# Performance work log

Hardware: AMD Instinct MI355X
Metric: run time of the kernel (lower is better)

## Reference

```python
import jax, jax.numpy as jnp
import numpy as np

DIM = 300
VOCAB = 50000
B = 16
T_ART = 2000   # divisible by lcm(1,2,4,10,25)=100 -> no remainder branch in ContractExpand
T_Q = 30
T_OPT = 16
RANGES = (1, 2, 4, 10, 25)


def setup_inputs():
    key = jax.random.key(0)
    ks = jax.random.split(key, 32)
    s = 1.0 / np.sqrt(DIM)
    n = lambda i, shape, scale: jax.random.normal(ks[i], shape, jnp.float32) * scale
    return {
        "option1_in": jax.random.randint(ks[0], (B, T_OPT), 0, VOCAB),
        "option2_in": jax.random.randint(ks[1], (B, T_OPT), 0, VOCAB),
        "option3_in": jax.random.randint(ks[2], (B, T_OPT), 0, VOCAB),
        "option4_in": jax.random.randint(ks[3], (B, T_OPT), 0, VOCAB),
        "question_in": jax.random.randint(ks[4], (B, T_Q), 0, VOCAB),
        "article_in": jax.random.randint(ks[5], (B, T_ART), 0, VOCAB),
        "emb": n(6, (VOCAB, DIM), 0.1),
        # ContractExpand: 5 range-specific DIM->DIM linears
        "ce_W": n(7, (5, DIM, DIM), s),
        "ce_b": n(8, (5, DIM), 0.01),
        # MultiRangedReasoning gate mixers: 5->3 and 3->1
        "mr1_W": n(9, (3, 5), 0.4),
        "mr1_b": n(10, (3,), 0.01),
        "mr2_W": n(11, (1, 3), 0.05),   # small scale keeps gate < 1 so 2000-step scan is stable
        "mr2_b": jnp.zeros((1,), jnp.float32),
        # MRU encoding linears
        "Wz": n(12, (DIM, DIM), s), "bz": n(13, (DIM,), 0.01),
        "Wo": n(14, (DIM, DIM), s), "bo": n(15, (DIM,), 0.01),
        # BiAttention key projections
        "f1_W": n(16, (DIM, DIM), s), "f1_b": n(17, (DIM,), 0.01),
        "f2_W": n(18, (DIM, DIM), s), "f2_b": n(19, (DIM,), 0.01),
        "f3_W": n(20, (DIM, DIM), s), "f3_b": n(21, (DIM,), 0.01),
        # AnswerSelection: 2*DIM -> DIM/4 -> 1
        "as1_W": n(22, (DIM // 4, 2 * DIM), 1.0 / np.sqrt(2 * DIM)),
        "as1_b": n(23, (DIM // 4,), 0.01),
        "as2_W": n(24, (1, DIM // 4), 1.0 / np.sqrt(DIM // 4)),
        "as2_b": n(25, (1,), 0.01),
    }


def _attention(main, attn_in, W, b):
    # score[b,t,w] = (W @ attn_in[b,w] + b) . main[b,t]; softmax over w; mix attn_in
    keys = attn_in @ W.T + b                               # (B,Tw,D)
    probs = jax.nn.softmax(jnp.einsum('btd,bwd->btw', main, keys), axis=-1)
    return jnp.einsum('btw,bwd->btd', probs, attn_in)      # (B,Tt,D)


def _forward(option1_in, option2_in, option3_in, option4_in, question_in, article_in,
             emb, ce_W, ce_b, mr1_W, mr1_b, mr2_W, mr2_b, Wz, bz, Wo, bo,
             f1_W, f1_b, f2_W, f2_b, f3_W, f3_b, as1_W, as1_b, as2_W, as2_b):
    art = emb[article_in]                                  # (B,T,D)
    q = emb[question_in]                                   # (B,Tq,D)
    opts = [emb[o] for o in (option1_in, option2_in, option3_in, option4_in)]

    # --- MultiRangedReasoning gate ---
    blocks = []
    for i, r in enumerate(RANGES):
        g = T_ART // r
        xs = art.reshape(B, g, r, DIM).sum(2)              # group-sum over r consecutive words
        h = jax.nn.relu(jnp.einsum('bgd,ed->bge', xs, ce_W[i]) + ce_b[i])
        blocks.append(jnp.repeat(h, r, axis=1) / r)        # expand back to (B,T,D)
    Y = jnp.stack(blocks, axis=-1)                         # (B,T,D,5)
    h1 = jax.nn.relu(jnp.einsum('btdr,kr->btdk', Y, mr1_W) + mr1_b)
    gate = jax.nn.relu(jnp.einsum('btdk,ok->btdo', h1, mr2_W) + mr2_b)[..., 0]  # (B,T,D)

    # --- MRU encoding: c_t = g_t*c_{t-1} + (1-g_t)*z_t ; h_t = o_t*c_t ---
    z = jnp.tanh(art @ Wz.T + bz)
    o = jnp.tanh(art @ Wo.T + bo)

    def step(c, gz):
        g_t, z_t = gz
        c = g_t * c + (1.0 - g_t) * z_t
        return c, c

    _, cs = jax.lax.scan(step, jnp.zeros((B, DIM), art.dtype),
                         (gate.transpose(1, 0, 2), z.transpose(1, 0, 2)))
    art_enc = o * cs.transpose(1, 0, 2)                    # (B,T,D)

    # --- bi-attention + per-option answer vector ---
    aoq = _attention(art_enc, q, f1_W, f1_b)               # article on question
    vecs = []
    for opt in opts:
        aoqo = _attention(aoq, opt, f2_W, f2_b)            # (B,T,D)
        ooa = _attention(aoq, opt, f3_W, f3_b)             # (B,T,D)
        vecs.append(jnp.concatenate([aoqo.mean(1), ooa.mean(1)], axis=-1))  # (B,2D)
    ans = jnp.stack(vecs, 0)                               # (4,B,2D)

    h = jax.nn.relu(ans @ as1_W.T + as1_b)                 # (4,B,75)
    scores = (h @ as2_W.T + as2_b)[..., 0]                 # (4,B)
    return scores.T                                        # (B,4)


def reference(option1_in, option2_in, option3_in, option4_in, question_in, article_in,
              emb, ce_W, ce_b, mr1_W, mr1_b, mr2_W, mr2_b, Wz, bz, Wo, bo,
              f1_W, f1_b, f2_W, f2_b, f3_W, f3_b, as1_W, as1_b, as2_W, as2_b):
    return _forward(option1_in, option2_in, option3_in, option4_in, question_in, article_in,
                    emb, ce_W, ce_b, mr1_W, mr1_b, mr2_W, mr2_b, Wz, bz, Wo, bo,
                    f1_W, f1_b, f2_W, f2_b, f3_W, f3_b, as1_W, as1_b, as2_W, as2_b)
```

## Files before the change

### kernel.cpp

```cpp
#include <hip/hip_runtime.h>
#include <math.h>

typedef unsigned short ushortT;
typedef short bf8 __attribute__((ext_vector_type(8)));
typedef float f32x4 __attribute__((ext_vector_type(4)));
typedef unsigned short us4 __attribute__((ext_vector_type(4)));

__device__ __forceinline__ float bf2f(ushortT u){
    union { unsigned int i; float f; } v; v.i = ((unsigned int)u) << 16; return v.f;
}
__device__ __forceinline__ ushortT f2bf(float f){
    union { float f; unsigned int i; } v; v.f = f;
    unsigned int x = v.i;
    return (ushortT)((x + 0x7fffu + ((x >> 16) & 1u)) >> 16);
}
__device__ __forceinline__ float4 f4add(float4 a, float4 b){
    return make_float4(a.x + b.x, a.y + b.y, a.z + b.z, a.w + b.w);
}


constexpr size_t OFF_ART   = 0;
constexpr size_t OFF_R2    = 9600000;
constexpr size_t OFF_GATE  = 19200000;
constexpr size_t OFF_HC    = 28800000;
constexpr size_t OFF_WB    = 37344000;
constexpr size_t OFF_QEMB  = 38024960;
constexpr size_t OFF_KEYSQ = 38168960;
constexpr size_t OFF_OPTE  = 38312960;
constexpr size_t OFF_KEYS2 = 38620160;
constexpr size_t OFF_KEYS3 = 38927360;
constexpr size_t OFF_SCANA = 39234560;
constexpr size_t OFF_SCANB = 39426560;
constexpr size_t OFF_CST   = 39618560;
constexpr size_t OFF_PART  = 39810560;
constexpr size_t OFF_MALL  = 39939584;



__global__ void k_pack(float* ws, const float* ceW, const float* Wz, const float* Wo){
    int id = blockIdx.x * 256 + threadIdx.x;
    if (id >= 680960) return;
    int m = id / 97280; int rr = id % 97280;
    int kt = rr / 9728; rr %= 9728;
    int nt = rr / 512;  rr %= 512;
    int lane = rr / 8; int j = rr % 8;
    int d = kt * 32 + (lane >> 4) * 8 + j;
    int e = nt * 16 + (lane & 15);
    float w = 0.f;
    if (d < 300 && e < 300) {
        const float* src = (m < 5) ? (ceW + (size_t)m * 90000) : (m == 5 ? Wz : Wo);
        w = src[(size_t)e * 300 + d];
    }
    ushortT hi = f2bf(w);
    ushortT lo = f2bf(w - bf2f(hi));
    ushortT* wb = (ushortT*)(ws + OFF_WB);
    wb[((size_t)(m * 20 + kt) * 19 + nt) * 512 + lane * 8 + j] = hi;
    wb[((size_t)(m * 20 + 10 + kt) * 19 + nt) * 512 + lane * 8 + j] = lo;
}

__device__ __forceinline__ bf8 load_bfrag(const ushortT* wb, int mp, int kt, int nt, int lane){
    return *(const bf8*)(wb + (((size_t)(mp + kt) * 19 + nt) * 512 + lane * 8));
}
__device__ __forceinline__ bf8 lds_afrag(const ushortT* LA, int tile, int kt, int part, int lane){
    return *(const bf8*)(LA + ((tile * 10 + kt) * 2 + part) * 512 + lane * 8);
}
__device__ __forceinline__ void lds_store_split(ushortT* LA, int r, int dc4, float4 s){
    int kt = dc4 / 8;
    int kk = (dc4 % 8) * 4;
    int quad = kk / 8, j = kk % 8;
    int lane = quad * 16 + (r & 15), tile = r >> 4;
    us4 h, l;
    h.x = f2bf(s.x); l.x = f2bf(s.x - bf2f(h.x));
    h.y = f2bf(s.y); l.y = f2bf(s.y - bf2f(h.y));
    h.z = f2bf(s.z); l.z = f2bf(s.z - bf2f(h.z));
    h.w = f2bf(s.w); l.w = f2bf(s.w - bf2f(h.w));
    int base = ((tile * 10 + kt) * 2) * 512 + lane * 8 + j;
    *(us4*)&LA[base] = h;
    *(us4*)&LA[base + 512] = l;
}
__device__ __forceinline__ void lds_zero_kt9(ushortT* LA, int tid){
    for (int i = tid; i < 1024; i += 256) {
        int sl = i >> 8, u = i & 255;
        int slice = (sl < 2) ? (18 + sl) : (36 + sl);
        *(unsigned int*)&LA[slice * 512 + u * 2] = 0u;
    }
}

__global__ void k_gather(float* ws, const float* emb, const int* art_in, const int* q_in,
                         const int* o1, const int* o2, const int* o3, const int* o4){
    size_t id = (size_t)blockIdx.x * 256 + threadIdx.x;
    const float4* embv = (const float4*)emb;
    if (id < 2400000) {
        size_t row = id / 75; int wi = (int)(id % 75);
        ((float4*)(ws + OFF_ART))[id] = embv[(size_t)art_in[row] * 75 + wi];
    } else if (id < 2436000) {
        size_t i2 = id - 2400000; size_t row = i2 / 75; int wi = (int)(i2 % 75);
        ((float4*)(ws + OFF_QEMB))[i2] = embv[(size_t)q_in[row] * 75 + wi];
    } else if (id < 2512800) {
        size_t i3 = id - 2436000; size_t row = i3 / 75; int wi = (int)(i3 % 75);
        int opt = (int)(row / 256); int rr = (int)(row % 256);
        const int* op = (opt == 0) ? o1 : (opt == 1) ? o2 : (opt == 2) ? o3 : o4;
        ((float4*)(ws + OFF_OPTE))[i3] = embv[(size_t)op[rr] * 75 + wi];
    }
}

__global__ void k_s2s5(float* ws){
    size_t id = (size_t)blockIdx.x * 256 + threadIdx.x;
    const float4* art = (const float4*)(ws + OFF_ART);
    if (id < 1200000) {
        size_t row = id / 75; int wi = (int)(id % 75);
        size_t b = row / 1000, g = row % 1000;
        const float4* p = art + ((b * 2000 + g * 2) * 75 + wi);
        ((float4*)(ws + OFF_GATE))[row * 75 + wi] = f4add(p[0], p[75]);
    } else if (id < 1680000) {
        size_t i2 = id - 1200000;
        size_t row = i2 / 75; int wi = (int)(i2 % 75);
        size_t b = row / 400, g = row % 400;
        const float4* p = art + ((b * 2000 + g * 5) * 75 + wi);
        float4 s = f4add(f4add(p[0], p[75]), f4add(p[150], p[225]));
        s = f4add(s, p[300]);
        ((float4*)(ws + OFF_R2))[row * 75 + wi] = s;
    }
}

__global__ __launch_bounds__(256) void k_ce_coarse(float* ws, const float* ceb){
    int gb = blockIdx.x;
    int kind, rows0, wi, rowLocal0;
    if (gb < 40)       { kind = 3; rows0 = 27200; wi = 4; rowLocal0 = gb * 32; }
    else if (gb < 140) { kind = 2; rows0 = 24000; wi = 3; rowLocal0 = (gb - 40) * 32; }
    else if (gb < 390) { kind = 1; rows0 = 16000; wi = 2; rowLocal0 = (gb - 140) * 32; }
    else               { kind = 0; rows0 = 0;     wi = 1; rowLocal0 = (gb - 390) * 32; }

    __shared__ ushortT LA[20480];
    int tid = threadIdx.x;
    lds_zero_kt9(LA, tid);
    __syncthreads();
    const float4* S2v = (const float4*)(ws + OFF_GATE);
    const float4* S5v = (const float4*)(ws + OFF_R2);
    for (int v = tid; v < 2400; v += 256) {
        int r = v / 75, dc4 = v % 75;
        int R = rowLocal0 + r;
        float4 s;
        if (kind == 0) {
            s = S2v[(size_t)R * 75 + dc4];
        } else if (kind == 1) {
            int b = R / 500, g = R % 500;
            const float4* p = S2v + ((size_t)b * 1000 + 2 * g) * 75 + dc4;
            s = f4add(p[0], p[75]);
        } else if (kind == 2) {
            int b = R / 200, g = R % 200;
            const float4* p = S5v + ((size_t)b * 400 + 2 * g) * 75 + dc4;
            s = f4add(p[0], p[75]);
        } else {
            int b = R / 80, g = R % 80;
            const float4* p = S5v + ((size_t)b * 400 + 5 * g) * 75 + dc4;
            s = f4add(f4add(p[0], p[75]), f4add(p[150], p[225]));
            s = f4add(s, p[300]);
        }
        lds_store_split(LA, r, dc4, s);
    }
    __syncthreads();

    int lane = tid & 63, wv = tid >> 6;
    int mrow = lane & 15, quad = lane >> 4;
    const ushortT* wb = (const ushortT*)(ws + OFF_WB);
    int mpH = wi * 20, mpL = wi * 20 + 10;

    for (int p = 0; p < 3; p++) {
        int n0 = wv + p * 8; if (n0 >= 19) break;
        int n1 = n0 + 4; bool has1 = (n1 < 19);
        f32x4 acc[2][2] = {{{0.f,0.f,0.f,0.f},{0.f,0.f,0.f,0.f}},
                           {{0.f,0.f,0.f,0.f},{0.f,0.f,0.f,0.f}}};
        #pragma unroll
        for (int kt = 0; kt < 10; kt++) {
            bf8 Ah0 = lds_afrag(LA, 0, kt, 0, lane), Al0 = lds_afrag(LA, 0, kt, 1, lane);
            bf8 Ah1 = lds_afrag(LA, 1, kt, 0, lane), Al1 = lds_afrag(LA, 1, kt, 1, lane);
            bf8 Bh = load_bfrag(wb, mpH, kt, n0, lane);
            bf8 Bl = load_bfrag(wb, mpL, kt, n0, lane);
            acc[0][0] = __builtin_amdgcn_mfma_f32_16x16x32_bf16(Ah0, Bh, acc[0][0], 0, 0, 0);
            acc[0][0] = __builtin_amdgcn_mfma_f32_16x16x32_bf16(Ah0, Bl, acc[0][0], 0, 0, 0);
            acc[0][0] = __builtin_amdgcn_mfma_f32_16x16x32_bf16(Al0, Bh, acc[0][0], 0, 0, 0);
            acc[0][1] = __builtin_amdgcn_mfma_f32_16x16x32_bf16(Ah1, Bh, acc[0][1], 0, 0, 0);
            acc[0][1] = __builtin_amdgcn_mfma_f32_16x16x32_bf16(Ah1, Bl, acc[0][1], 0, 0, 0);
            acc[0][1] = __builtin_amdgcn_mfma_f32_16x16x32_bf16(Al1, Bh, acc[0][1], 0, 0, 0);
            if (has1) {
                bf8 Bh1 = load_bfrag(wb, mpH, kt, n1, lane);
                bf8 Bl1 = load_bfrag(wb, mpL, kt, n1, lane);
                acc[1][0] = __builtin_amdgcn_mfma_f32_16x16x32_bf16(Ah0, Bh1, acc[1][0], 0, 0, 0);
                acc[1][0] = __builtin_amdgcn_mfma_f32_16x16x32_bf16(Ah0, Bl1, acc[1][0], 0, 0, 0);
                acc[1][0] = __builtin_amdgcn_mfma_f32_16x16x32_bf16(Al0, Bh1, acc[1][0], 0, 0, 0);
                acc[1][1] = __builtin_amdgcn_mfma_f32_16x16x32_bf16(Ah1, Bh1, acc[1][1], 0, 0, 0);
                acc[1][1] = __builtin_amdgcn_mfma_f32_16x16x32_bf16(Ah1, Bl1, acc[1][1], 0, 0, 0);
                acc[1][1] = __builtin_amdgcn_mfma_f32_16x16x32_bf16(Al1, Bh1, acc[1][1], 0, 0, 0);
            }
        }
        #pragma unroll
        for (int ni = 0; ni < 2; ni++) {
            int nt = ni ? n1 : n0;
            if (ni && !has1) break;
            int e = nt * 16 + mrow;
            if (e >= 300) continue;
            float bv = ceb[wi * 300 + e];
            #pragma unroll
            for (int tile = 0; tile < 2; tile++)
                #pragma unroll
                for (int q = 0; q < 4; q++) {
                    int row = rows0 + rowLocal0 + tile * 16 + quad * 4 + q;
                    ws[OFF_HC + (size_t)row * 300 + e] = fmaxf(acc[ni][tile][q] + bv, 0.f);
                }
        }
    }
}

__global__ __launch_bounds__(256) void k_fused(float* ws, const float* ceb,
                                               const float* m1W, const float* m1b,
                                               const float* m2W, const float* m2b,
                                               const float* bz){
    int row0 = blockIdx.x * 32;
    __shared__ ushortT LA[20480];
    int tid = threadIdx.x;
    lds_zero_kt9(LA, tid);
    __syncthreads();
    for (int v = tid; v < 2400; v += 256) {
        int r = v / 75, dc4 = v % 75;
        float4 s = *(const float4*)&ws[OFF_ART + (size_t)(row0 + r) * 300 + dc4 * 4];
        lds_store_split(LA, r, dc4, s);
    }
    __syncthreads();

    float w1[3][5], b1[3], w2[3], b2;
    #pragma unroll
    for (int k = 0; k < 3; k++) {
        #pragma unroll
        for (int i = 0; i < 5; i++) w1[k][i] = m1W[k * 5 + i];
        b1[k] = m1b[k]; w2[k] = m2W[k];
    }
    b2 = m2b[0];

    int lane = tid & 63, wv = tid >> 6;
    int mrow = lane & 15, quad = lane >> 4;
    const ushortT* wb = (const ushortT*)(ws + OFF_WB);

    for (int p = 0; p < 3; p++) {
        int n0 = wv + p * 8; if (n0 >= 19) break;
        int n1 = n0 + 4; bool has1 = (n1 < 19);
        f32x4 aA[2][2] = {{{0.f,0.f,0.f,0.f},{0.f,0.f,0.f,0.f}},
                          {{0.f,0.f,0.f,0.f},{0.f,0.f,0.f,0.f}}};
        f32x4 aZ[2][2] = {{{0.f,0.f,0.f,0.f},{0.f,0.f,0.f,0.f}},
                          {{0.f,0.f,0.f,0.f},{0.f,0.f,0.f,0.f}}};
        #pragma unroll
        for (int kt = 0; kt < 10; kt++) {
            bf8 Ah0 = lds_afrag(LA, 0, kt, 0, lane), Al0 = lds_afrag(LA, 0, kt, 1, lane);
            bf8 Ah1 = lds_afrag(LA, 1, kt, 0, lane), Al1 = lds_afrag(LA, 1, kt, 1, lane);
            {
                bf8 B0h = load_bfrag(wb, 0,   kt, n0, lane);
                bf8 B0l = load_bfrag(wb, 10,  kt, n0, lane);
                bf8 B5h = load_bfrag(wb, 100, kt, n0, lane);
                bf8 B5l = load_bfrag(wb, 110, kt, n0, lane);
                aA[0][0] = __builtin_amdgcn_mfma_f32_16x16x32_bf16(Ah0, B0h, aA[0][0], 0, 0, 0);
                aZ[0][0] = __builtin_amdgcn_mfma_f32_16x16x32_bf16(Ah0, B5h, aZ[0][0], 0, 0, 0);
                aA[0][0] = __builtin_amdgcn_mfma_f32_16x16x32_bf16(Ah0, B0l, aA[0][0], 0, 0, 0);
                aZ[0][0] = __builtin_amdgcn_mfma_f32_16x16x32_bf16(Ah0, B5l, aZ[0][0], 0, 0, 0);
                aA[0][0] = __builtin_amdgcn_mfma_f32_16x16x32_bf16(Al0, B0h, aA[0][0], 0, 0, 0);
                aZ[0][0] = __builtin_amdgcn_mfma_f32_16x16x32_bf16(Al0, B5h, aZ[0][0], 0, 0, 0);
                aA[0][1] = __builtin_amdgcn_mfma_f32_16x16x32_bf16(Ah1, B0h, aA[0][1], 0, 0, 0);
                aZ[0][1] = __builtin_amdgcn_mfma_f32_16x16x32_bf16(Ah1, B5h, aZ[0][1], 0, 0, 0);
                aA[0][1] = __builtin_amdgcn_mfma_f32_16x16x32_bf16(Ah1, B0l, aA[0][1], 0, 0, 0);
                aZ[0][1] = __builtin_amdgcn_mfma_f32_16x16x32_bf16(Ah1, B5l, aZ[0][1], 0, 0, 0);
                aA[0][1] = __builtin_amdgcn_mfma_f32_16x16x32_bf16(Al1, B0h, aA[0][1], 0, 0, 0);
                aZ[0][1] = __builtin_amdgcn_mfma_f32_16x16x32_bf16(Al1, B5h, aZ[0][1], 0, 0, 0);
            }
            if (has1) {
                bf8 B0h = load_bfrag(wb, 0,   kt, n1, lane);
                bf8 B0l = load_bfrag(wb, 10,  kt, n1, lane);
                bf8 B5h = load_bfrag(wb, 100, kt, n1, lane);
                bf8 B5l = load_bfrag(wb, 110, kt, n1, lane);
                aA[1][0] = __builtin_amdgcn_mfma_f32_16x16x32_bf16(Ah0, B0h, aA[1][0], 0, 0, 0);
                aZ[1][0] = __builtin_amdgcn_mfma_f32_16x16x32_bf16(Ah0, B5h, aZ[1][0], 0, 0, 0);
                aA[1][0] = __builtin_amdgcn_mfma_f32_16x16x32_bf16(Ah0, B0l, aA[1][0], 0, 0, 0);
                aZ[1][0] = __builtin_amdgcn_mfma_f32_16x16x32_bf16(Ah0, B5l, aZ[1][0], 0, 0, 0);
                aA[1][0] = __builtin_amdgcn_mfma_f32_16x16x32_bf16(Al0, B0h, aA[1][0], 0, 0, 0);
                aZ[1][0] = __builtin_amdgcn_mfma_f32_16x16x32_bf16(Al0, B5h, aZ[1][0], 0, 0, 0);
                aA[1][1] = __builtin_amdgcn_mfma_f32_16x16x32_bf16(Ah1, B0h, aA[1][1], 0, 0, 0);
                aZ[1][1] = __builtin_amdgcn_mfma_f32_16x16x32_bf16(Ah1, B5h, aZ[1][1], 0, 0, 0);
                aA[1][1] = __builtin_amdgcn_mfma_f32_16x16x32_bf16(Ah1, B0l, aA[1][1], 0, 0, 0);
                aZ[1][1] = __builtin_amdgcn_mfma_f32_16x16x32_bf16(Ah1, B5l, aZ[1][1], 0, 0, 0);
                aA[1][1] = __builtin_amdgcn_mfma_f32_16x16x32_bf16(Al1, B0h, aA[1][1], 0, 0, 0);
                aZ[1][1] = __builtin_amdgcn_mfma_f32_16x16x32_bf16(Al1, B5h, aZ[1][1], 0, 0, 0);
            }
        }
        #pragma unroll
        for (int ni = 0; ni < 2; ni++) {
            if (ni && !has1) break;
            int nt = ni ? n1 : n0;
            int e = nt * 16 + mrow;
            if (e >= 300) continue;
            float cebe = ceb[e], bze = bz[e];
            #pragma unroll
            for (int tile = 0; tile < 2; tile++) {
                #pragma unroll
                for (int q = 0; q < 4; q++) {
                    int row = row0 + tile * 16 + quad * 4 + q;
                    int bb = row / 2000, t = row % 2000;
                    size_t c1 = OFF_HC + ((size_t)bb * 1000 + t / 2) * 300;
                    size_t c2 = OFF_HC + (16000 + (size_t)bb * 500 + t / 4) * 300;
                    size_t c3 = OFF_HC + (24000 + (size_t)bb * 200 + t / 10) * 300;
                    size_t c4 = OFF_HC + (27200 + (size_t)bb * 80 + t / 25) * 300;
                    float y0 = fmaxf(aA[ni][tile][q] + cebe, 0.f);
                    float y1 = ws[c1 + e] * 0.5f;
                    float y2 = ws[c2 + e] * 0.25f;
                    float y3 = ws[c3 + e] * 0.1f;
                    float y4 = ws[c4 + e] * 0.04f;
                    float gacc = b2;
                    #pragma unroll
                    for (int k = 0; k < 3; k++) {
                        float a = b1[k] + y0 * w1[k][0] + y1 * w1[k][1] + y2 * w1[k][2]
                                + y3 * w1[k][3] + y4 * w1[k][4];
                        gacc += fmaxf(a, 0.f) * w2[k];
                    }
                    ws[OFF_GATE + (size_t)row * 300 + e] = fmaxf(gacc, 0.f);
                    ws[OFF_R2 + (size_t)row * 300 + e] = tanhf(aZ[ni][tile][q] + bze);
                }
            }
        }
    }
}

__global__ void k_scan1(float* ws){
    int tid = blockIdx.x * 256 + threadIdx.x;
    if (tid >= 192000) return;
    int c = tid / 4800, ch = tid % 4800;
    int b = ch / 300, d = ch % 300;
    size_t base = (size_t)b * 2000 * 300 + d;
    float A = 1.f, Bv = 0.f;
    int t0 = c * 50;
    for (int k = 0; k < 50; k++) {
        size_t ix = base + (size_t)(t0 + k) * 300;
        float g = ws[OFF_GATE + ix], zz = ws[OFF_R2 + ix];
        Bv = g * Bv + (1.f - g) * zz;
        A *= g;
    }
    ws[OFF_SCANA + tid] = A;
    ws[OFF_SCANB + tid] = Bv;
}

__global__ void k_scan2(float* ws){
    int ch = blockIdx.x * 256 + threadIdx.x;
    if (ch >= 4800) return;
    float c = 0.f;
    for (int j = 0; j < 40; j++) {
        ws[OFF_CST + (size_t)j * 4800 + ch] = c;
        c = ws[OFF_SCANA + (size_t)j * 4800 + ch] * c + ws[OFF_SCANB + (size_t)j * 4800 + ch];
    }
}

__global__ void k_scan3(float* ws){
    int tid = blockIdx.x * 256 + threadIdx.x;
    if (tid >= 192000) return;
    int c = tid / 4800, ch = tid % 4800;
    int b = ch / 300, d = ch % 300;
    size_t base = (size_t)b * 2000 * 300 + d;
    float cc = ws[OFF_CST + tid];
    int t0 = c * 50;
    for (int k = 0; k < 50; k++) {
        size_t ix = base + (size_t)(t0 + k) * 300;
        float g = ws[OFF_GATE + ix], zz = ws[OFF_R2 + ix];
        cc = g * cc + (1.f - g) * zz;
        ws[OFF_R2 + ix] = cc;
    }
}

__global__ __launch_bounds__(256) void k_oenc(float* ws, const float* bo){
    int row0 = blockIdx.x * 32;
    __shared__ ushortT LA[20480];
    int tid = threadIdx.x;
    lds_zero_kt9(LA, tid);
    __syncthreads();
    for (int v = tid; v < 2400; v += 256) {
        int r = v / 75, dc4 = v % 75;
        float4 s = *(const float4*)&ws[OFF_ART + (size_t)(row0 + r) * 300 + dc4 * 4];
        lds_store_split(LA, r, dc4, s);
    }
    __syncthreads();

    int lane = tid & 63, wv = tid >> 6;
    int mrow = lane & 15, quad = lane >> 4;
    const ushortT* wb = (const ushortT*)(ws + OFF_WB);

    for (int p = 0; p < 3; p++) {
        int n0 = wv + p * 8; if (n0 >= 19) break;
        int n1 = n0 + 4; bool has1 = (n1 < 19);
        f32x4 acc[2][2] = {{{0.f,0.f,0.f,0.f},{0.f,0.f,0.f,0.f}},
                           {{0.f,0.f,0.f,0.f},{0.f,0.f,0.f,0.f}}};
        #pragma unroll
        for (int kt = 0; kt < 10; kt++) {
            bf8 Ah0 = lds_afrag(LA, 0, kt, 0, lane), Al0 = lds_afrag(LA, 0, kt, 1, lane);
            bf8 Ah1 = lds_afrag(LA, 1, kt, 0, lane), Al1 = lds_afrag(LA, 1, kt, 1, lane);
            bf8 Bh = load_bfrag(wb, 120, kt, n0, lane);
            bf8 Bl = load_bfrag(wb, 130, kt, n0, lane);
            acc[0][0] = __builtin_amdgcn_mfma_f32_16x16x32_bf16(Ah0, Bh, acc[0][0], 0, 0, 0);
            acc[0][0] = __builtin_amdgcn_mfma_f32_16x16x32_bf16(Ah0, Bl, acc[0][0], 0, 0, 0);
            acc[0][0] = __builtin_amdgcn_mfma_f32_16x16x32_bf16(Al0, Bh, acc[0][0], 0, 0, 0);
            acc[0][1] = __builtin_amdgcn_mfma_f32_16x16x32_bf16(Ah1, Bh, acc[0][1], 0, 0, 0);
            acc[0][1] = __builtin_amdgcn_mfma_f32_16x16x32_bf16(Ah1, Bl, acc[0][1], 0, 0, 0);
            acc[0][1] = __builtin_amdgcn_mfma_f32_16x16x32_bf16(Al1, Bh, acc[0][1], 0, 0, 0);
            if (has1) {
                bf8 Bh1 = load_bfrag(wb, 120, kt, n1, lane);
                bf8 Bl1 = load_bfrag(wb, 130, kt, n1, lane);
                acc[1][0] = __builtin_amdgcn_mfma_f32_16x16x32_bf16(Ah0, Bh1, acc[1][0], 0, 0, 0);
                acc[1][0] = __builtin_amdgcn_mfma_f32_16x16x32_bf16(Ah0, Bl1, acc[1][0], 0, 0, 0);
                acc[1][0] = __builtin_amdgcn_mfma_f32_16x16x32_bf16(Al0, Bh1, acc[1][0], 0, 0, 0);
                acc[1][1] = __builtin_amdgcn_mfma_f32_16x16x32_bf16(Ah1, Bh1, acc[1][1], 0, 0, 0);
                acc[1][1] = __builtin_amdgcn_mfma_f32_16x16x32_bf16(Ah1, Bl1, acc[1][1], 0, 0, 0);
                acc[1][1] = __builtin_amdgcn_mfma_f32_16x16x32_bf16(Al1, Bh1, acc[1][1], 0, 0, 0);
            }
        }
        #pragma unroll
        for (int ni = 0; ni < 2; ni++) {
            if (ni && !has1) break;
            int nt = ni ? n1 : n0;
            int e = nt * 16 + mrow;
            if (e >= 300) continue;
            float bv = bo[e];
            #pragma unroll
            for (int tile = 0; tile < 2; tile++)
                #pragma unroll
                for (int q = 0; q < 4; q++) {
                    size_t idx = OFF_R2 + (size_t)(row0 + tile * 16 + quad * 4 + q) * 300 + e;
                    ws[idx] = tanhf(acc[ni][tile][q] + bv) * ws[idx];
                }
        }
    }
}

__global__ __launch_bounds__(320) void k_keys(float* ws, const float* f1W, const float* f1b,
                                              const float* f2W, const float* f2b,
                                              const float* f3W, const float* f3b){
    int rid = blockIdx.x;
    const float* src; const float* W; const float* bias; float* out;
    if (rid < 480)       { src = ws + OFF_QEMB + (size_t)rid * 300;               W = f1W; bias = f1b; out = ws + OFF_KEYSQ + (size_t)rid * 300; }
    else if (rid < 1504) { int rr = rid - 480;  src = ws + OFF_OPTE + (size_t)rr * 300; W = f2W; bias = f2b; out = ws + OFF_KEYS2 + (size_t)rr * 300; }
    else                 { int rr = rid - 1504; src = ws + OFF_OPTE + (size_t)rr * 300; W = f3W; bias = f3b; out = ws + OFF_KEYS3 + (size_t)rr * 300; }
    __shared__ float X[300];
    int tid = threadIdx.x;
    for (int i = tid; i < 300; i += 320) X[i] = src[i];
    __syncthreads();
    if (tid < 300) {
        float acc = bias[tid];
        const float* wr = W + (size_t)tid * 300;
        for (int d = 0; d < 300; d++) acc += X[d] * wr[d];
        out[tid] = acc;
    }
}

__global__ __launch_bounds__(256) void k_matt(float* ws){
    int b = blockIdx.x;
    __shared__ float Q[30 * 300];
    int tid = threadIdx.x;
    for (int v = tid; v < 2250; v += 256)
        *(float4*)&Q[v * 4] = *(const float4*)&ws[OFF_QEMB + (size_t)b * 9000 + (size_t)v * 4];
    __syncthreads();
    int cw = tid & 127, half = tid >> 7;
    int combo = cw >> 4, w = cw & 15;
    size_t kbase = (combo < 4)
        ? OFF_KEYS2 + ((size_t)combo * 256 + (size_t)b * 16 + w) * 300
        : OFF_KEYS3 + ((size_t)(combo - 4) * 256 + (size_t)b * 16 + w) * 300;
    const float4* kr = (const float4*)&ws[kbase];
    for (int wp = half * 15; wp < half * 15 + 15; wp++) {
        const float4* qr = (const float4*)&Q[wp * 300];
        float a = 0.f;
        #pragma unroll 5
        for (int j = 0; j < 75; j++) {
            float4 k = kr[j], q = qr[j];
            a += k.x * q.x + k.y * q.y + k.z * q.z + k.w * q.w;
        }
        ws[OFF_MALL + (size_t)b * 3840 + (size_t)wp * 128 + cw] = a;
    }
}

__global__ __launch_bounds__(256) void k_attn(float* ws){
    int tile = blockIdx.x, b = blockIdx.y;
    int t0 = tile * 32;
    __shared__ __align__(16) float U[9728];
    __shared__ float S[32 * 30];
    int tid = threadIdx.x;

    for (int v = tid; v < 2432; v += 256) {
        int r = v / 76, c = v % 76;
        int t = t0 + r;
        float4 val = make_float4(0.f, 0.f, 0.f, 0.f);
        if (c < 75 && t < 2000)
            val = *(const float4*)&ws[OFF_R2 + ((size_t)b * 2000 + t) * 300 + (size_t)c * 4];
        *(float4*)&U[r * 304 + c * 4] = val;
    }
    __syncthreads();

    if (tid < 240) {
        int q = tid / 30, w = tid % 30;
        const float4* kr = (const float4*)&ws[OFF_KEYSQ + (size_t)b * 9000 + (size_t)w * 300];
        const float4* x0 = (const float4*)&U[(q * 4 + 0) * 304];
        const float4* x1 = (const float4*)&U[(q * 4 + 1) * 304];
        const float4* x2 = (const float4*)&U[(q * 4 + 2) * 304];
        const float4* x3 = (const float4*)&U[(q * 4 + 3) * 304];
        float a0 = 0.f, a1 = 0.f, a2 = 0.f, a3 = 0.f;
// ... 76 lines not shown
    const float* oe = ws + OFF_OPTE + ((size_t)o * 256 + (size_t)b * 16) * 300;
    for (int idx = tid; idx < 600; idx += 256) {
        int half = idx / 300, e = idx % 300;
        float acc = 0.f;
        for (int w = 0; w < 16; w++) acc += cm[half * 16 + w] * oe[(size_t)w * 300 + e];
        vec[idx] = acc;
    }
    __syncthreads();
    if (tid < 75) {
        float acc = as1b[tid];
        for (int m = 0; m < 600; m++) acc += vec[m] * as1W[(size_t)tid * 600 + m];
        hb[tid] = fmaxf(acc, 0.f);
    }
    __syncthreads();
    if (tid == 0) {
        float s = as2b[0];
        for (int j = 0; j < 75; j++) s += hb[j] * as2W[j];
        out[b * 4 + o] = s;
    }
}

extern "C" void kernel_launch(void* const* d_in, const int* in_sizes, int n_in,
                              void* d_out, int out_size, void* d_ws, size_t ws_size,
                              hipStream_t stream) {
    float* ws = (float*)d_ws;
    const int* o1 = (const int*)d_in[0];
    const int* o2 = (const int*)d_in[1];
    const int* o3 = (const int*)d_in[2];
    const int* o4 = (const int*)d_in[3];
    const int* qin = (const int*)d_in[4];
    const int* ain = (const int*)d_in[5];
    const float* emb  = (const float*)d_in[6];
    const float* ceW  = (const float*)d_in[7];
    const float* ceb  = (const float*)d_in[8];
    const float* m1W  = (const float*)d_in[9];
    const float* m1b  = (const float*)d_in[10];
    const float* m2W  = (const float*)d_in[11];
    const float* m2b  = (const float*)d_in[12];
    const float* Wz   = (const float*)d_in[13];
    const float* bz   = (const float*)d_in[14];
    const float* Wo   = (const float*)d_in[15];
    const float* bo   = (const float*)d_in[16];
    const float* f1W  = (const float*)d_in[17];
    const float* f1b  = (const float*)d_in[18];
    const float* f2W  = (const float*)d_in[19];
    const float* f2b  = (const float*)d_in[20];
    const float* f3W  = (const float*)d_in[21];
    const float* f3b  = (const float*)d_in[22];
    const float* as1W = (const float*)d_in[23];
    const float* as1b = (const float*)d_in[24];
    const float* as2W = (const float*)d_in[25];
    const float* as2b = (const float*)d_in[26];

    k_pack<<<(680960 + 255) / 256, 256, 0, stream>>>(ws, ceW, Wz, Wo);
    k_gather<<<(2512800 + 255) / 256, 256, 0, stream>>>(ws, emb, ain, qin, o1, o2, o3, o4);
    k_s2s5<<<(1680000 + 255) / 256, 256, 0, stream>>>(ws);
    k_ce_coarse<<<890, 256, 0, stream>>>(ws, ceb);
    k_fused<<<1000, 256, 0, stream>>>(ws, ceb, m1W, m1b, m2W, m2b, bz);
    k_scan1<<<750, 256, 0, stream>>>(ws);
    k_scan2<<<19, 256, 0, stream>>>(ws);
    k_scan3<<<750, 256, 0, stream>>>(ws);
    k_oenc<<<1000, 256, 0, stream>>>(ws, bo);
    k_keys<<<2528, 320, 0, stream>>>(ws, f1W, f1b, f2W, f2b, f3W, f3b);
    k_matt<<<16, 256, 0, stream>>>(ws);
    k_attn<<<dim3(63, 16), 256, 0, stream>>>(ws);
    k_final<<<64, 256, 0, stream>>>(ws, as1W, as1b, as2W, as2b, (float*)d_out);
}
```

Before: 645.3 us.

## Fuse gather with pooled sums, fold output encoding into fused GEMM, MFMA key projections

```diff
diff --git a/kernel.cpp b/kernel.cpp
--- a/kernel.cpp
+++ b/kernel.cpp
@@ -24,22 +24,23 @@
 constexpr size_t OFF_GATE  = 19200000;
 constexpr size_t OFF_HC    = 28800000;
 constexpr size_t OFF_WB    = 37344000;
-constexpr size_t OFF_QEMB  = 38024960;
-constexpr size_t OFF_KEYSQ = 38168960;
-constexpr size_t OFF_OPTE  = 38312960;
-constexpr size_t OFF_KEYS2 = 38620160;
-constexpr size_t OFF_KEYS3 = 38927360;
-constexpr size_t OFF_SCANA = 39234560;
-constexpr size_t OFF_SCANB = 39426560;
-constexpr size_t OFF_CST   = 39618560;
-constexpr size_t OFF_PART  = 39810560;
-constexpr size_t OFF_MALL  = 39939584;
-
-
-
-__global__ void k_pack(float* ws, const float* ceW, const float* Wz, const float* Wo){
+constexpr size_t OFF_QEMB  = 38316800;
+constexpr size_t OFF_KEYSQ = 38460800;
+constexpr size_t OFF_OPTE  = 38604800;
+constexpr size_t OFF_KEYS2 = 38912000;
+constexpr size_t OFF_KEYS3 = 39219200;
+constexpr size_t OFF_SCANA = 39526400;
+constexpr size_t OFF_SCANB = 39718400;
+constexpr size_t OFF_CST   = 39910400;
+constexpr size_t OFF_PART  = 40102400;
+constexpr size_t OFF_MALL  = 40231424;
+
+
+
+__global__ void k_pack(float* ws, const float* ceW, const float* Wz, const float* Wo,
+                       const float* f1W, const float* f2W, const float* f3W){
     int id = blockIdx.x * 256 + threadIdx.x;
-    if (id >= 680960) return;
+    if (id >= 972800) return;
     int m = id / 97280; int rr = id % 97280;
     int kt = rr / 9728; rr %= 9728;
     int nt = rr / 512;  rr %= 512;
@@ -48,7 +49,9 @@
     int e = nt * 16 + (lane & 15);
     float w = 0.f;
     if (d < 300 && e < 300) {
-        const float* src = (m < 5) ? (ceW + (size_t)m * 90000) : (m == 5 ? Wz : Wo);
+        const float* src = (m < 5) ? (ceW + (size_t)m * 90000)
+                         : (m == 5) ? Wz : (m == 6) ? Wo
+                         : (m == 7) ? f1W : (m == 8) ? f2W : f3W;
         w = src[(size_t)e * 300 + d];
     }
     ushortT hi = f2bf(w);
@@ -86,40 +89,40 @@
     }
 }
 
-__global__ void k_gather(float* ws, const float* emb, const int* art_in, const int* q_in,
+__global__ __launch_bounds__(320) void k_gather2(float* ws, const float* emb,
+                         const int* art_in, const int* q_in,
                          const int* o1, const int* o2, const int* o3, const int* o4){
-    size_t id = (size_t)blockIdx.x * 256 + threadIdx.x;
+    int gb = blockIdx.x, tid = threadIdx.x;
     const float4* embv = (const float4*)emb;
-    if (id < 2400000) {
-        size_t row = id / 75; int wi = (int)(id % 75);
-        ((float4*)(ws + OFF_ART))[id] = embv[(size_t)art_in[row] * 75 + wi];
-    } else if (id < 2436000) {
-        size_t i2 = id - 2400000; size_t row = i2 / 75; int wi = (int)(i2 % 75);
-        ((float4*)(ws + OFF_QEMB))[i2] = embv[(size_t)q_in[row] * 75 + wi];
-    } else if (id < 2512800) {
-        size_t i3 = id - 2436000; size_t row = i3 / 75; int wi = (int)(i3 % 75);
-        int opt = (int)(row / 256); int rr = (int)(row % 256);
-        const int* op = (opt == 0) ? o1 : (opt == 1) ? o2 : (opt == 2) ? o3 : o4;
-        ((float4*)(ws + OFF_OPTE))[i3] = embv[(size_t)op[rr] * 75 + wi];
-    }
-}
-
-__global__ void k_s2s5(float* ws){
-    size_t id = (size_t)blockIdx.x * 256 + threadIdx.x;
-    const float4* art = (const float4*)(ws + OFF_ART);
-    if (id < 1200000) {
-        size_t row = id / 75; int wi = (int)(id % 75);
-        size_t b = row / 1000, g = row % 1000;
-        const float4* p = art + ((b * 2000 + g * 2) * 75 + wi);
-        ((float4*)(ws + OFF_GATE))[row * 75 + wi] = f4add(p[0], p[75]);
-    } else if (id < 1680000) {
-        size_t i2 = id - 1200000;
-        size_t row = i2 / 75; int wi = (int)(i2 % 75);
-        size_t b = row / 400, g = row % 400;
-        const float4* p = art + ((b * 2000 + g * 5) * 75 + wi);
-        float4 s = f4add(f4add(p[0], p[75]), f4add(p[150], p[225]));
-        s = f4add(s, p[300]);
-        ((float4*)(ws + OFF_R2))[row * 75 + wi] = s;
+    if (gb < 160) {
+        if (tid >= 300) return;
+        int b = gb / 10, c = gb % 10;
+        int rg = tid / 75, d4 = tid % 75;
+        int tbase = c * 200 + rg * 50;
+        float4 s2 = make_float4(0.f,0.f,0.f,0.f), s5 = s2;
+        float4* artv  = (float4*)(ws + OFF_ART);
+        float4* s2v   = (float4*)(ws + OFF_GATE);
+        float4* s5v   = (float4*)(ws + OFF_R2);
+        for (int i = 0; i < 50; i++) {
+            int t = tbase + i;
+            int tok = art_in[b * 2000 + t];
+            float4 v = embv[(size_t)tok * 75 + d4];
+            artv[((size_t)b * 2000 + t) * 75 + d4] = v;
+            s2 = f4add(s2, v); s5 = f4add(s5, v);
+            if ((i & 1) == 1) { s2v[((size_t)b * 1000 + (t >> 1)) * 75 + d4] = s2; s2 = make_float4(0.f,0.f,0.f,0.f); }
+            if (i % 5 == 4)   { s5v[((size_t)b * 400 + t / 5) * 75 + d4] = s5;   s5 = make_float4(0.f,0.f,0.f,0.f); }
+        }
+    } else {
+        int id = (gb - 160) * 320 + tid;
+        if (id < 36000) {
+            size_t row = id / 75; int wi = id % 75;
+            ((float4*)(ws + OFF_QEMB))[id] = embv[(size_t)q_in[row] * 75 + wi];
+        } else if (id < 112800) {
+            int i3 = id - 36000; size_t row = i3 / 75; int wi = i3 % 75;
+            int opt = (int)(row / 256); int rr = (int)(row % 256);
+            const int* op = (opt == 0) ? o1 : (opt == 1) ? o2 : (opt == 2) ? o3 : o4;
+            ((float4*)(ws + OFF_OPTE))[i3] = embv[(size_t)op[rr] * 75 + wi];
+        }
     }
 }
 
@@ -166,48 +169,31 @@
     const ushortT* wb = (const ushortT*)(ws + OFF_WB);
     int mpH = wi * 20, mpL = wi * 20 + 10;
 
-    for (int p = 0; p < 3; p++) {
-        int n0 = wv + p * 8; if (n0 >= 19) break;
-        int n1 = n0 + 4; bool has1 = (n1 < 19);
-        f32x4 acc[2][2] = {{{0.f,0.f,0.f,0.f},{0.f,0.f,0.f,0.f}},
-                           {{0.f,0.f,0.f,0.f},{0.f,0.f,0.f,0.f}}};
+    for (int p = 0; p < 5; p++) {
+        int nt = wv + p * 4; if (nt >= 19) break;
+        f32x4 a0 = {0.f,0.f,0.f,0.f}, a1 = {0.f,0.f,0.f,0.f};
         #pragma unroll
         for (int kt = 0; kt < 10; kt++) {
             bf8 Ah0 = lds_afrag(LA, 0, kt, 0, lane), Al0 = lds_afrag(LA, 0, kt, 1, lane);
             bf8 Ah1 = lds_afrag(LA, 1, kt, 0, lane), Al1 = lds_afrag(LA, 1, kt, 1, lane);
-            bf8 Bh = load_bfrag(wb, mpH, kt, n0, lane);
-            bf8 Bl = load_bfrag(wb, mpL, kt, n0, lane);
-            acc[0][0] = __builtin_amdgcn_mfma_f32_16x16x32_bf16(Ah0, Bh, acc[0][0], 0, 0, 0);
-            acc[0][0] = __builtin_amdgcn_mfma_f32_16x16x32_bf16(Ah0, Bl, acc[0][0], 0, 0, 0);
-            acc[0][0] = __builtin_amdgcn_mfma_f32_16x16x32_bf16(Al0, Bh, acc[0][0], 0, 0, 0);
-            acc[0][1] = __builtin_amdgcn_mfma_f32_16x16x32_bf16(Ah1, Bh, acc[0][1], 0, 0, 0);
-            acc[0][1] = __builtin_amdgcn_mfma_f32_16x16x32_bf16(Ah1, Bl, acc[0][1], 0, 0, 0);
-            acc[0][1] = __builtin_amdgcn_mfma_f32_16x16x32_bf16(Al1, Bh, acc[0][1], 0, 0, 0);
-            if (has1) {
-                bf8 Bh1 = load_bfrag(wb, mpH, kt, n1, lane);
-                bf8 Bl1 = load_bfrag(wb, mpL, kt, n1, lane);
-                acc[1][0] = __builtin_amdgcn_mfma_f32_16x16x32_bf16(Ah0, Bh1, acc[1][0], 0, 0, 0);
-                acc[1][0] = __builtin_amdgcn_mfma_f32_16x16x32_bf16(Ah0, Bl1, acc[1][0], 0, 0, 0);
-                acc[1][0] = __builtin_amdgcn_mfma_f32_16x16x32_bf16(Al0, Bh1, acc[1][0], 0, 0, 0);
-                acc[1][1] = __builtin_amdgcn_mfma_f32_16x16x32_bf16(Ah1, Bh1, acc[1][1], 0, 0, 0);
-                acc[1][1] = __builtin_amdgcn_mfma_f32_16x16x32_bf16(Ah1, Bl1, acc[1][1], 0, 0, 0);
-                acc[1][1] = __builtin_amdgcn_mfma_f32_16x16x32_bf16(Al1, Bh1, acc[1][1], 0, 0, 0);
-            }
-        }
-        #pragma unroll
-        for (int ni = 0; ni < 2; ni++) {
-            int nt = ni ? n1 : n0;
-            if (ni && !has1) break;
-            int e = nt * 16 + mrow;
-            if (e >= 300) continue;
+            bf8 Bh = load_bfrag(wb, mpH, kt, nt, lane);
+            bf8 Bl = load_bfrag(wb, mpL, kt, nt, lane);
+            a0 = __builtin_amdgcn_mfma_f32_16x16x32_bf16(Ah0, Bh, a0, 0, 0, 0);
+            a1 = __builtin_amdgcn_mfma_f32_16x16x32_bf16(Ah1, Bh, a1, 0, 0, 0);
+            a0 = __builtin_amdgcn_mfma_f32_16x16x32_bf16(Ah0, Bl, a0, 0, 0, 0);
+            a1 = __builtin_amdgcn_mfma_f32_16x16x32_bf16(Ah1, Bl, a1, 0, 0, 0);
+            a0 = __builtin_amdgcn_mfma_f32_16x16x32_bf16(Al0, Bh, a0, 0, 0, 0);
+            a1 = __builtin_amdgcn_mfma_f32_16x16x32_bf16(Al1, Bh, a1, 0, 0, 0);
+        }
+        int e = nt * 16 + mrow;
+        if (e < 300) {
             float bv = ceb[wi * 300 + e];
             #pragma unroll
-            for (int tile = 0; tile < 2; tile++)
-                #pragma unroll
-                for (int q = 0; q < 4; q++) {
-                    int row = rows0 + rowLocal0 + tile * 16 + quad * 4 + q;
-                    ws[OFF_HC + (size_t)row * 300 + e] = fmaxf(acc[ni][tile][q] + bv, 0.f);
-                }
+            for (int q = 0; q < 4; q++) {
+                int r0 = rows0 + rowLocal0 + quad * 4 + q;
+                ws[OFF_HC + (size_t)r0 * 300 + e] = fmaxf(a0[q] + bv, 0.f);
+                ws[OFF_HC + (size_t)(r0 + 16) * 300 + e] = fmaxf(a1[q] + bv, 0.f);
+            }
         }
     }
 }
@@ -215,7 +201,7 @@
 __global__ __launch_bounds__(256) void k_fused(float* ws, const float* ceb,
                                                const float* m1W, const float* m1b,
                                                const float* m2W, const float* m2b,
-                                               const float* bz){
+                                               const float* bz, const float* bo){
     int row0 = blockIdx.x * 32;
     __shared__ ushortT LA[20480];
     int tid = threadIdx.x;
@@ -241,72 +227,56 @@
     int mrow = lane & 15, quad = lane >> 4;
     const ushortT* wb = (const ushortT*)(ws + OFF_WB);
 
-    for (int p = 0; p < 3; p++) {
-        int n0 = wv + p * 8; if (n0 >= 19) break;
-        int n1 = n0 + 4; bool has1 = (n1 < 19);
-        f32x4 aA[2][2] = {{{0.f,0.f,0.f,0.f},{0.f,0.f,0.f,0.f}},
-                          {{0.f,0.f,0.f,0.f},{0.f,0.f,0.f,0.f}}};
-        f32x4 aZ[2][2] = {{{0.f,0.f,0.f,0.f},{0.f,0.f,0.f,0.f}},
-                          {{0.f,0.f,0.f,0.f},{0.f,0.f,0.f,0.f}}};
+    for (int p = 0; p < 5; p++) {
+        int nt = wv + p * 4; if (nt >= 19) break;
+        f32x4 aA0 = {0.f,0.f,0.f,0.f}, aA1 = aA0;
+        f32x4 aZ0 = aA0, aZ1 = aA0, aO0 = aA0, aO1 = aA0;
         #pragma unroll
         for (int kt = 0; kt < 10; kt++) {
             bf8 Ah0 = lds_afrag(LA, 0, kt, 0, lane), Al0 = lds_afrag(LA, 0, kt, 1, lane);
             bf8 Ah1 = lds_afrag(LA, 1, kt, 0, lane), Al1 = lds_afrag(LA, 1, kt, 1, lane);
-            {
-                bf8 B0h = load_bfrag(wb, 0,   kt, n0, lane);
-                bf8 B0l = load_bfrag(wb, 10,  kt, n0, lane);
-                bf8 B5h = load_bfrag(wb, 100, kt, n0, lane);
-                bf8 B5l = load_bfrag(wb, 110, kt, n0, lane);
-                aA[0][0] = __builtin_amdgcn_mfma_f32_16x16x32_bf16(Ah0, B0h, aA[0][0], 0, 0, 0);
-                aZ[0][0] = __builtin_amdgcn_mfma_f32_16x16x32_bf16(Ah0, B5h, aZ[0][0], 0, 0, 0);
-                aA[0][0] = __builtin_amdgcn_mfma_f32_16x16x32_bf16(Ah0, B0l, aA[0][0], 0, 0, 0);
-                aZ[0][0] = __builtin_amdgcn_mfma_f32_16x16x32_bf16(Ah0, B5l, aZ[0][0], 0, 0, 0);
-                aA[0][0] = __builtin_amdgcn_mfma_f32_16x16x32_bf16(Al0, B0h, aA[0][0], 0, 0, 0);
-                aZ[0][0] = __builtin_amdgcn_mfma_f32_16x16x32_bf16(Al0, B5h, aZ[0][0], 0, 0, 0);
-                aA[0][1] = __builtin_amdgcn_mfma_f32_16x16x32_bf16(Ah1, B0h, aA[0][1], 0, 0, 0);
-                aZ[0][1] = __builtin_amdgcn_mfma_f32_16x16x32_bf16(Ah1, B5h, aZ[0][1], 0, 0, 0);
-                aA[0][1] = __builtin_amdgcn_mfma_f32_16x16x32_bf16(Ah1, B0l, aA[0][1], 0, 0, 0);
-                aZ[0][1] = __builtin_amdgcn_mfma_f32_16x16x32_bf16(Ah1, B5l, aZ[0][1], 0, 0, 0);
-                aA[0][1] = __builtin_amdgcn_mfma_f32_16x16x32_bf16(Al1, B0h, aA[0][1], 0, 0, 0);
-                aZ[0][1] = __builtin_amdgcn_mfma_f32_16x16x32_bf16(Al1, B5h, aZ[0][1], 0, 0, 0);
-            }
-            if (has1) {
-                bf8 B0h = load_bfrag(wb, 0,   kt, n1, lane);
-                bf8 B0l = load_bfrag(wb, 10,  kt, n1, lane);
-                bf8 B5h = load_bfrag(wb, 100, kt, n1, lane);
-                bf8 B5l = load_bfrag(wb, 110, kt, n1, lane);
-                aA[1][0] = __builtin_amdgcn_mfma_f32_16x16x32_bf16(Ah0, B0h, aA[1][0], 0, 0, 0);
-                aZ[1][0] = __builtin_amdgcn_mfma_f32_16x16x32_bf16(Ah0, B5h, aZ[1][0], 0, 0, 0);
-                aA[1][0] = __builtin_amdgcn_mfma_f32_16x16x32_bf16(Ah0, B0l, aA[1][0], 0, 0, 0);
-                aZ[1][0] = __builtin_amdgcn_mfma_f32_16x16x32_bf16(Ah0, B5l, aZ[1][0], 0, 0, 0);
-                aA[1][0] = __builtin_amdgcn_mfma_f32_16x16x32_bf16(Al0, B0h, aA[1][0], 0, 0, 0);
-                aZ[1][0] = __builtin_amdgcn_mfma_f32_16x16x32_bf16(Al0, B5h, aZ[1][0], 0, 0, 0);
-                aA[1][1] = __builtin_amdgcn_mfma_f32_16x16x32_bf16(Ah1, B0h, aA[1][1], 0, 0, 0);
-                aZ[1][1] = __builtin_amdgcn_mfma_f32_16x16x32_bf16(Ah1, B5h, aZ[1][1], 0, 0, 0);
-                aA[1][1] = __builtin_amdgcn_mfma_f32_16x16x32_bf16(Ah1, B0l, aA[1][1], 0, 0, 0);
-                aZ[1][1] = __builtin_amdgcn_mfma_f32_16x16x32_bf16(Ah1, B5l, aZ[1][1], 0, 0, 0);
-                aA[1][1] = __builtin_amdgcn_mfma_f32_16x16x32_bf16(Al1, B0h, aA[1][1], 0, 0, 0);
-                aZ[1][1] = __builtin_amdgcn_mfma_f32_16x16x32_bf16(Al1, B5h, aZ[1][1], 0, 0, 0);
-            }
-        }
-        #pragma unroll
-        for (int ni = 0; ni < 2; ni++) {
-            if (ni && !has1) break;
-            int nt = ni ? n1 : n0;
-            int e = nt * 16 + mrow;
-            if (e >= 300) continue;
-            float cebe = ceb[e], bze = bz[e];
+            bf8 BAh = load_bfrag(wb, 0,   kt, nt, lane);
+            bf8 BAl = load_bfrag(wb, 10,  kt, nt, lane);
+            bf8 BZh = load_bfrag(wb, 100, kt, nt, lane);
+            bf8 BZl = load_bfrag(wb, 110, kt, nt, lane);
+            bf8 BOh = load_bfrag(wb, 120, kt, nt, lane);
+            bf8 BOl = load_bfrag(wb, 130, kt, nt, lane);
+            aA0 = __builtin_amdgcn_mfma_f32_16x16x32_bf16(Ah0, BAh, aA0, 0, 0, 0);
+            aZ0 = __builtin_amdgcn_mfma_f32_16x16x32_bf16(Ah0, BZh, aZ0, 0, 0, 0);
+            aO0 = __builtin_amdgcn_mfma_f32_16x16x32_bf16(Ah0, BOh, aO0, 0, 0, 0);
+            aA1 = __builtin_amdgcn_mfma_f32_16x16x32_bf16(Ah1, BAh, aA1, 0, 0, 0);
+            aZ1 = __builtin_amdgcn_mfma_f32_16x16x32_bf16(Ah1, BZh, aZ1, 0, 0, 0);
+            aO1 = __builtin_amdgcn_mfma_f32_16x16x32_bf16(Ah1, BOh, aO1, 0, 0, 0);
+            aA0 = __builtin_amdgcn_mfma_f32_16x16x32_bf16(Ah0, BAl, aA0, 0, 0, 0);
+            aZ0 = __builtin_amdgcn_mfma_f32_16x16x32_bf16(Ah0, BZl, aZ0, 0, 0, 0);
+            aO0 = __builtin_amdgcn_mfma_f32_16x16x32_bf16(Ah0, BOl, aO0, 0, 0, 0);
+            aA1 = __builtin_amdgcn_mfma_f32_16x16x32_bf16(Ah1, BAl, aA1, 0, 0, 0);
+            aZ1 = __builtin_amdgcn_mfma_f32_16x16x32_bf16(Ah1, BZl, aZ1, 0, 0, 0);
+            aO1 = __builtin_amdgcn_mfma_f32_16x16x32_bf16(Ah1, BOl, aO1, 0, 0, 0);
+            aA0 = __builtin_amdgcn_mfma_f32_16x16x32_bf16(Al0, BAh, aA0, 0, 0, 0);
+            aZ0 = __builtin_amdgcn_mfma_f32_16x16x32_bf16(Al0, BZh, aZ0, 0, 0, 0);
+            aO0 = __builtin_amdgcn_mfma_f32_16x16x32_bf16(Al0, BOh, aO0, 0, 0, 0);
+            aA1 = __builtin_amdgcn_mfma_f32_16x16x32_bf16(Al1, BAh, aA1, 0, 0, 0);
+            aZ1 = __builtin_amdgcn_mfma_f32_16x16x32_bf16(Al1, BZh, aZ1, 0, 0, 0);
+            aO1 = __builtin_amdgcn_mfma_f32_16x16x32_bf16(Al1, BOh, aO1, 0, 0, 0);
+        }
+        int e = nt * 16 + mrow;
+        if (e < 300) {
+            float cebe = ceb[e], bze = bz[e], boe = bo[e];
             #pragma unroll
             for (int tile = 0; tile < 2; tile++) {
                 #pragma unroll
                 for (int q = 0; q < 4; q++) {
+                    float vA = tile ? aA1[q] : aA0[q];
+                    float vZ = tile ? aZ1[q] : aZ0[q];
+                    float vO = tile ? aO1[q] : aO0[q];
                     int row = row0 + tile * 16 + quad * 4 + q;
                     int bb = row / 2000, t = row % 2000;
                     size_t c1 = OFF_HC + ((size_t)bb * 1000 + t / 2) * 300;
                     size_t c2 = OFF_HC + (16000 + (size_t)bb * 500 + t / 4) * 300;
                     size_t c3 = OFF_HC + (24000 + (size_t)bb * 200 + t / 10) * 300;
                     size_t c4 = OFF_HC + (27200 + (size_t)bb * 80 + t / 25) * 300;
-                    float y0 = fmaxf(aA[ni][tile][q] + cebe, 0.f);
+                    float y0 = fmaxf(vA + cebe, 0.f);
                     float y1 = ws[c1 + e] * 0.5f;
                     float y2 = ws[c2 + e] * 0.25f;
                     float y3 = ws[c3 + e] * 0.1f;
@@ -319,7 +289,8 @@
                         gacc += fmaxf(a, 0.f) * w2[k];
                     }
                     ws[OFF_GATE + (size_t)row * 300 + e] = fmaxf(gacc, 0.f);
-                    ws[OFF_R2 + (size_t)row * 300 + e] = tanhf(aZ[ni][tile][q] + bze);
+                    ws[OFF_R2 + (size_t)row * 300 + e] = tanhf(vZ + bze);
+                    ws[OFF_ART + (size_t)row * 300 + e] = tanhf(vO + boe);
                 }
             }
         }
@@ -366,19 +337,25 @@
         size_t ix = base + (size_t)(t0 + k) * 300;
         float g = ws[OFF_GATE + ix], zz = ws[OFF_R2 + ix];
         cc = g * cc + (1.f - g) * zz;
-        ws[OFF_R2 + ix] = cc;
-    }
-}
-
-__global__ __launch_bounds__(256) void k_oenc(float* ws, const float* bo){
-    int row0 = blockIdx.x * 32;
+        ws[OFF_R2 + ix] = ws[OFF_ART + ix] * cc;
+    }
+}
+
+__global__ __launch_bounds__(256) void k_keysm(float* ws, const float* f1b,
+                                               const float* f2b, const float* f3b){
+    int gb = blockIdx.x;
+    int wm, rowLocal0; size_t inoff, outoff; const float* bias;
+    if (gb < 15)      { wm = 7; inoff = OFF_QEMB; outoff = OFF_KEYSQ; bias = f1b; rowLocal0 = gb * 32; }
+    else if (gb < 47) { wm = 8; inoff = OFF_OPTE; outoff = OFF_KEYS2; bias = f2b; rowLocal0 = (gb - 15) * 32; }
+    else              { wm = 9; inoff = OFF_OPTE; outoff = OFF_KEYS3; bias = f3b; rowLocal0 = (gb - 47) * 32; }
+
     __shared__ ushortT LA[20480];
     int tid = threadIdx.x;
     lds_zero_kt9(LA, tid);
     __syncthreads();
     for (int v = tid; v < 2400; v += 256) {
         int r = v / 75, dc4 = v % 75;
-        float4 s = *(const float4*)&ws[OFF_ART + (size_t)(row0 + r) * 300 + dc4 * 4];
+        float4 s = *(const float4*)&ws[inoff + (size_t)(rowLocal0 + r) * 300 + dc4 * 4];
         lds_store_split(LA, r, dc4, s);
     }
     __syncthreads();
@@ -386,70 +363,34 @@
     int lane = tid & 63, wv = tid >> 6;
     int mrow = lane & 15, quad = lane >> 4;
     const ushortT* wb = (const ushortT*)(ws + OFF_WB);
-
-    for (int p = 0; p < 3; p++) {
-        int n0 = wv + p * 8; if (n0 >= 19) break;
-        int n1 = n0 + 4; bool has1 = (n1 < 19);
-        f32x4 acc[2][2] = {{{0.f,0.f,0.f,0.f},{0.f,0.f,0.f,0.f}},
-                           {{0.f,0.f,0.f,0.f},{0.f,0.f,0.f,0.f}}};
+    int mpH = wm * 20, mpL = wm * 20 + 10;
+
+    for (int p = 0; p < 5; p++) {
+        int nt = wv + p * 4; if (nt >= 19) break;
+        f32x4 a0 = {0.f,0.f,0.f,0.f}, a1 = {0.f,0.f,0.f,0.f};
         #pragma unroll
         for (int kt = 0; kt < 10; kt++) {
             bf8 Ah0 = lds_afrag(LA, 0, kt, 0, lane), Al0 = lds_afrag(LA, 0, kt, 1, lane);
             bf8 Ah1 = lds_afrag(LA, 1, kt, 0, lane), Al1 = lds_afrag(LA, 1, kt, 1, lane);
-            bf8 Bh = load_bfrag(wb, 120, kt, n0, lane);
-            bf8 Bl = load_bfrag(wb, 130, kt, n0, lane);
-            acc[0][0] = __builtin_amdgcn_mfma_f32_16x16x32_bf16(Ah0, Bh, acc[0][0], 0, 0, 0);
-            acc[0][0] = __builtin_amdgcn_mfma_f32_16x16x32_bf16(Ah0, Bl, acc[0][0], 0, 0, 0);
-            acc[0][0] = __builtin_amdgcn_mfma_f32_16x16x32_bf16(Al0, Bh, acc[0][0], 0, 0, 0);
-            acc[0][1] = __builtin_amdgcn_mfma_f32_16x16x32_bf16(Ah1, Bh, acc[0][1], 0, 0, 0);
-            acc[0][1] = __builtin_amdgcn_mfma_f32_16x16x32_bf16(Ah1, Bl, acc[0][1], 0, 0, 0);
-            acc[0][1] = __builtin_amdgcn_mfma_f32_16x16x32_bf16(Al1, Bh, acc[0][1], 0, 0, 0);
-            if (has1) {
-                bf8 Bh1 = load_bfrag(wb, 120, kt, n1, lane);
-                bf8 Bl1 = load_bfrag(wb, 130, kt, n1, lane);
-                acc[1][0] = __builtin_amdgcn_mfma_f32_16x16x32_bf16(Ah0, Bh1, acc[1][0], 0, 0, 0);
-                acc[1][0] = __builtin_amdgcn_mfma_f32_16x16x32_bf16(Ah0, Bl1, acc[1][0], 0, 0, 0);
-                acc[1][0] = __builtin_amdgcn_mfma_f32_16x16x32_bf16(Al0, Bh1, acc[1][0], 0, 0, 0);
-                acc[1][1] = __builtin_amdgcn_mfma_f32_16x16x32_bf16(Ah1, Bh1, acc[1][1], 0, 0, 0);
-                acc[1][1] = __builtin_amdgcn_mfma_f32_16x16x32_bf16(Ah1, Bl1, acc[1][1], 0, 0, 0);
-                acc[1][1] = __builtin_amdgcn_mfma_f32_16x16x32_bf16(Al1, Bh1, acc[1][1], 0, 0, 0);
+            bf8 Bh = load_bfrag(wb, mpH, kt, nt, lane);
+            bf8 Bl = load_bfrag(wb, mpL, kt, nt, lane);
+            a0 = __builtin_amdgcn_mfma_f32_16x16x32_bf16(Ah0, Bh, a0, 0, 0, 0);
+            a1 = __builtin_amdgcn_mfma_f32_16x16x32_bf16(Ah1, Bh, a1, 0, 0, 0);
+            a0 = __builtin_amdgcn_mfma_f32_16x16x32_bf16(Ah0, Bl, a0, 0, 0, 0);
+            a1 = __builtin_amdgcn_mfma_f32_16x16x32_bf16(Ah1, Bl, a1, 0, 0, 0);
+            a0 = __builtin_amdgcn_mfma_f32_16x16x32_bf16(Al0, Bh, a0, 0, 0, 0);
+            a1 = __builtin_amdgcn_mfma_f32_16x16x32_bf16(Al1, Bh, a1, 0, 0, 0);
+        }
+        int e = nt * 16 + mrow;
+        if (e < 300) {
+            float bv = bias[e];
+            #pragma unroll
+            for (int q = 0; q < 4; q++) {
+                int r0 = rowLocal0 + quad * 4 + q;
+                ws[outoff + (size_t)r0 * 300 + e] = a0[q] + bv;
+                ws[outoff + (size_t)(r0 + 16) * 300 + e] = a1[q] + bv;
             }
         }
-        #pragma unroll
-        for (int ni = 0; ni < 2; ni++) {
-            if (ni && !has1) break;
-            int nt = ni ? n1 : n0;
-            int e = nt * 16 + mrow;
-            if (e >= 300) continue;
-            float bv = bo[e];
-            #pragma unroll
-            for (int tile = 0; tile < 2; tile++)
-                #pragma unroll
-                for (int q = 0; q < 4; q++) {
-                    size_t idx = OFF_R2 + (size_t)(row0 + tile * 16 + quad * 4 + q) * 300 + e;
-                    ws[idx] = tanhf(acc[ni][tile][q] + bv) * ws[idx];
-                }
-        }
-    }
-}
-
-__global__ __launch_bounds__(320) void k_keys(float* ws, const float* f1W, const float* f1b,
-                                              const float* f2W, const float* f2b,
-                                              const float* f3W, const float* f3b){
-    int rid = blockIdx.x;
-    const float* src; const float* W; const float* bias; float* out;
-    if (rid < 480)       { src = ws + OFF_QEMB + (size_t)rid * 300;               W = f1W; bias = f1b; out = ws + OFF_KEYSQ + (size_t)rid * 300; }
-    else if (rid < 1504) { int rr = rid - 480;  src = ws + OFF_OPTE + (size_t)rr * 300; W = f2W; bias = f2b; out = ws + OFF_KEYS2 + (size_t)rr * 300; }
-    else                 { int rr = rid - 1504; src = ws + OFF_OPTE + (size_t)rr * 300; W = f3W; bias = f3b; out = ws + OFF_KEYS3 + (size_t)rr * 300; }
-    __shared__ float X[300];
-    int tid = threadIdx.x;
-    for (int i = tid; i < 300; i += 320) X[i] = src[i];
-    __syncthreads();
-    if (tid < 300) {
-        float acc = bias[tid];
-        const float* wr = W + (size_t)tid * 300;
-        for (int d = 0; d < 300; d++) acc += X[d] * wr[d];
-        out[tid] = acc;
     }
 }
 
@@ -632,16 +573,14 @@
     const float* as2W = (const float*)d_in[25];
     const float* as2b = (const float*)d_in[26];
 
-    k_pack<<<(680960 + 255) / 256, 256, 0, stream>>>(ws, ceW, Wz, Wo);
-    k_gather<<<(2512800 + 255) / 256, 256, 0, stream>>>(ws, emb, ain, qin, o1, o2, o3, o4);
-    k_s2s5<<<(1680000 + 255) / 256, 256, 0, stream>>>(ws);
+    k_pack<<<3800, 256, 0, stream>>>(ws, ceW, Wz, Wo, f1W, f2W, f3W);
+    k_gather2<<<513, 320, 0, stream>>>(ws, emb, ain, qin, o1, o2, o3, o4);
     k_ce_coarse<<<890, 256, 0, stream>>>(ws, ceb);
-    k_fused<<<1000, 256, 0, stream>>>(ws, ceb, m1W, m1b, m2W, m2b, bz);
+    k_fused<<<1000, 256, 0, stream>>>(ws, ceb, m1W, m1b, m2W, m2b, bz, bo);
     k_scan1<<<750, 256, 0, stream>>>(ws);
     k_scan2<<<19, 256, 0, stream>>>(ws);
     k_scan3<<<750, 256, 0, stream>>>(ws);
-    k_oenc<<<1000, 256, 0, stream>>>(ws, bo);
-    k_keys<<<2528, 320, 0, stream>>>(ws, f1W, f1b, f2W, f2b, f3W, f3b);
+    k_keysm<<<79, 256, 0, stream>>>(ws, f1b, f2b, f3b);
     k_matt<<<16, 256, 0, stream>>>(ws);
     k_attn<<<dim3(63, 16), 256, 0, stream>>>(ws);
     k_final<<<64, 256, 0, stream>>>(ws, as1W, as1b, as2W, as2b, (float*)d_out);
```

Result: faster. 539.1 us (-16.5%).
